# Optimization experiments

Measured on AMD Instinct MI355X. Metric: run time of the kernel, lower is better.

The kernel has to match this reference:

```python
import jax, jax.numpy as jnp
import numpy as np

D_MODEL = 1024
N_HEADS = 16
D_K = D_MODEL // N_HEADS


def setup_inputs() -> dict:
    key = jax.random.key(0)
    ks = jax.random.split(key, 5)
    x = jax.random.normal(ks[0], (4, 2048, D_MODEL), dtype=jnp.float32)
    # nn.Linear stores weight as [out, in]; we store transposed [in, out] for x @ W
    w_qkv = jax.random.normal(ks[1], (D_MODEL, 3 * D_MODEL), dtype=jnp.float32) / np.sqrt(D_MODEL)
    b_qkv = jnp.zeros((3 * D_MODEL,), dtype=jnp.float32)
    w_fc = jax.random.normal(ks[2], (D_MODEL, D_MODEL), dtype=jnp.float32) / np.sqrt(D_MODEL)
    b_fc = jnp.zeros((D_MODEL,), dtype=jnp.float32)
    ln_g = jnp.ones((D_MODEL,), dtype=jnp.float32)
    ln_b = jnp.zeros((D_MODEL,), dtype=jnp.float32)
    return {"x": x, "w_qkv": w_qkv, "b_qkv": b_qkv, "w_fc": w_fc, "b_fc": b_fc,
            "ln_g": ln_g, "ln_b": ln_b}


def _layernorm(x, g, b, eps=1e-5):
    mu = jnp.mean(x, axis=-1, keepdims=True)
    var = jnp.mean(jnp.square(x - mu), axis=-1, keepdims=True)
    return (x - mu) * jax.lax.rsqrt(var + eps) * g + b


def reference(x, w_qkv, b_qkv, w_fc, b_fc, ln_g, ln_b):
    residual = x
    xn = _layernorm(x, ln_g, ln_b)
    B, L, D = xn.shape
    qkv = xn @ w_qkv + b_qkv  # [B, L, 3D]
    q, k, v = jnp.split(qkv, 3, axis=-1)
    # b l (h d) -> b h l d
    def to_heads(t):
        return t.reshape(B, L, N_HEADS, D_K).transpose(0, 2, 1, 3)
    q, k, v = to_heads(q), to_heads(k), to_heads(v)
    scale = 1.0 / np.sqrt(D_K)
    scores = jnp.einsum('bhld,bhmd->bhlm', q, k) * scale  # [B,H,L,L]
    attn = jax.nn.softmax(scores, axis=-1)
    # dropout is identity in eval mode
    out = jnp.einsum('bhlm,bhmd->bhld', attn, v)  # [B,H,L,d]
    out = out.transpose(0, 2, 1, 3).reshape(B, L, D)  # b h l d -> b l (h d)
    out = out @ w_fc + b_fc
    return out + residual
```

## Files before the change

kernel.cpp:

```cpp
#include <hip/hip_runtime.h>
#include <hip/hip_bf16.h>
#include <cstdint>
#include <cstddef>

using bf16 = __hip_bfloat16;
typedef __attribute__((ext_vector_type(4))) float f32x4;
typedef __attribute__((ext_vector_type(8))) short bf16x8;

#define D_MODEL 1024
#define SEQ     2048
#define NB      4
#define NHEAD   16
#define DHEAD   64
#define NROWS   (NB * SEQ)

__device__ __forceinline__ void load_lds16(const void* g, void* l) {
  __builtin_amdgcn_global_load_lds(
      (const __attribute__((address_space(1))) unsigned int*)g,
      (__attribute__((address_space(3))) unsigned int*)l, 16, 0, 0);
}

__device__ __forceinline__ unsigned short f2bf(float f) {
  bf16 h = __float2bfloat16(f);
  return *(unsigned short*)&h;
}

__device__ __forceinline__ unsigned pk_trunc(float a, float b) {
  union { float f; unsigned u; } ca, cb;
  ca.f = a; cb.f = b;
  return (ca.u >> 16) | (cb.u & 0xffff0000u);
}

__global__ __launch_bounds__(256) void ln_kernel(
    const float* __restrict__ x, const float* __restrict__ g,
    const float* __restrict__ bb, bf16* __restrict__ xn) {
  int row  = blockIdx.x * 4 + (threadIdx.x >> 6);
  int lane = threadIdx.x & 63;
  const float4* xr = (const float4*)(x + (size_t)row * D_MODEL);
  float v[16], s = 0.f;
#pragma unroll
  for (int i = 0; i < 4; i++) {
    float4 t = xr[lane + 64 * i];
    v[4 * i] = t.x; v[4 * i + 1] = t.y; v[4 * i + 2] = t.z; v[4 * i + 3] = t.w;
    s += t.x + t.y + t.z + t.w;
  }
#pragma unroll
  for (int off = 32; off; off >>= 1) s += __shfl_xor(s, off, 64);
  float mean = s * (1.f / D_MODEL);
  float vs = 0.f;
#pragma unroll
  for (int i = 0; i < 16; i++) { float d = v[i] - mean; vs += d * d; }
#pragma unroll
  for (int off = 32; off; off >>= 1) vs += __shfl_xor(vs, off, 64);
  float rstd = rsqrtf(vs * (1.f / D_MODEL) + 1e-5f);
  ushort4* op = (ushort4*)(xn + (size_t)row * D_MODEL);
#pragma unroll
  for (int i = 0; i < 4; i++) {
    float4 gv = ((const float4*)g)[lane + 64 * i];
    float4 bv = ((const float4*)bb)[lane + 64 * i];
    ushort4 o;
    o.x = f2bf((v[4 * i]     - mean) * rstd * gv.x + bv.x);
    o.y = f2bf((v[4 * i + 1] - mean) * rstd * gv.y + bv.y);
    o.z = f2bf((v[4 * i + 2] - mean) * rstd * gv.z + bv.z);
    o.w = f2bf((v[4 * i + 3] - mean) * rstd * gv.w + bv.w);
    op[lane + 64 * i] = o;
  }
}

__global__ __launch_bounds__(256) void transpose_kernel(
    const float* __restrict__ w_qkv, bf16* __restrict__ wqkvT,
    const float* __restrict__ w_fc, bf16* __restrict__ wfcT) {
  __shared__ float tile[32][33];
  const float* in; bf16* out; int C, c0;
  if (blockIdx.x < 96) { in = w_qkv; out = wqkvT; C = 3072; c0 = blockIdx.x * 32; }
  else                 { in = w_fc;  out = wfcT;  C = 1024; c0 = (blockIdx.x - 96) * 32; }
  int r0 = blockIdx.y * 32;
  int tx = threadIdx.x & 31, ty = threadIdx.x >> 5;
  for (int i = ty; i < 32; i += 8)
    tile[i][tx] = in[(size_t)(r0 + i) * C + c0 + tx];
  __syncthreads();
  for (int i = ty; i < 32; i += 8)
    out[(size_t)(c0 + i) * 1024 + r0 + tx] = __float2bfloat16(tile[tx][i]);
}

__device__ __forceinline__ void store_ct(bf16* p, float v)  { *p = __float2bfloat16(v); }
__device__ __forceinline__ void store_ct(float* p, float v) { *p = v; }

template <int SPLIT, int RESID, typename CT>
__global__ __launch_bounds__(256) void gemm_bt(
    const bf16* __restrict__ A, const bf16* __restrict__ Bt,
    const float* __restrict__ bias, const float* __restrict__ resid,
    CT* __restrict__ C, bf16* __restrict__ vt, int M, int N, int K) {
  __shared__ __attribute__((aligned(16))) bf16 Alds[128 * 64];
  __shared__ __attribute__((aligned(16))) bf16 Blds[128 * 64];
  int tid = threadIdx.x, wave = tid >> 6, lane = tid & 63;
  int ntiles = N >> 7;
  int bm = blockIdx.x / ntiles, bn = blockIdx.x % ntiles;
  int m0 = bm << 7, n0 = bn << 7;
  int wm = (wave >> 1) << 6, wn = (wave & 1) << 6;
  int srow = tid >> 3;
  int sw8  = (((tid & 7) ^ (srow & 7)) << 3);
  int frow = lane & 15, quad = lane >> 4;
  const bf16* Ap[4];
  const bf16* Bp[4];
#pragma unroll
  for (int s = 0; s < 4; s++) {
    Ap[s] = A  + (size_t)(m0 + s * 32 + srow) * K + sw8;
    Bp[s] = Bt + (size_t)(n0 + s * 32 + srow) * K + sw8;
  }
  f32x4 acc[4][4] = {};
  for (int k0 = 0; k0 < K; k0 += 64) {
    __syncthreads();
#pragma unroll
    for (int s = 0; s < 4; s++) {
      load_lds16(Ap[s], (char*)Alds + s * 4096 + tid * 16);
      load_lds16(Bp[s], (char*)Blds + s * 4096 + tid * 16);
      Ap[s] += 64; Bp[s] += 64;
    }
    __syncthreads();
    bf16x8 af[4][2], bv[4][2];
#pragma unroll
    for (int i = 0; i < 4; i++)
#pragma unroll
      for (int kk = 0; kk < 2; kk++) {
        int e = (((kk * 4 + quad) ^ (frow & 7)) << 3);
        af[i][kk] = *(const bf16x8*)&Alds[(wm + i * 16 + frow) * 64 + e];
        bv[i][kk] = *(const bf16x8*)&Blds[(wn + i * 16 + frow) * 64 + e];
      }
#pragma unroll
    for (int i = 0; i < 4; i++)
#pragma unroll
      for (int j = 0; j < 4; j++) {
        acc[i][j] = __builtin_amdgcn_mfma_f32_16x16x32_bf16(af[i][0], bv[j][0], acc[i][j], 0, 0, 0);
        acc[i][j] = __builtin_amdgcn_mfma_f32_16x16x32_bf16(af[i][1], bv[j][1], acc[i][j], 0, 0, 0);
      }
  }
#pragma unroll
  for (int i = 0; i < 4; i++) {
    int row0 = m0 + wm + i * 16 + (quad << 2);
#pragma unroll
    for (int j = 0; j < 4; j++) {
      int col = n0 + wn + j * 16 + frow;
      float bvs = bias[col];
      if (SPLIT && col >= 2048) {
        int hd = col - 2048;
        int b = row0 >> 11, seq0 = row0 & 2047;
        int within = seq0 & 63, mt = within >> 4, q4 = (within >> 2) & 3;
        int pos = (seq0 & ~63) + ((mt >> 1) << 5) + (q4 << 3) + ((mt & 1) << 2);
        ushort4 pk;
        pk.x = f2bf(acc[i][j][0] + bvs);
        pk.y = f2bf(acc[i][j][1] + bvs);
        pk.z = f2bf(acc[i][j][2] + bvs);
        pk.w = f2bf(acc[i][j][3] + bvs);
        *(ushort4*)&vt[((size_t)(b * 1024 + hd)) * SEQ + pos] = pk;
      } else {
        int stride = SPLIT ? 2048 : N;
        float scale = (SPLIT && col < 1024) ? 0.18033688f : 1.0f;
#pragma unroll
        for (int r = 0; r < 4; r++) {
          size_t idx = (size_t)(row0 + r) * stride + col;
          float val = (acc[i][j][r] + bvs) * scale;
          if (RESID) val += resid[idx];
          store_ct(&C[idx], val);
        }
      }
    }
  }
}

__global__ __launch_bounds__(256, 4) void attn_kernel(
    const bf16* __restrict__ qk, const bf16* __restrict__ vt,
    bf16* __restrict__ aout) {
  int bh = blockIdx.x;
  int qt = blockIdx.y;
  int bb = bh >> 4, h = bh & 15;
  const bf16* Qg = qk + (size_t)bb * SEQ * 2048 + h * DHEAD;
  const bf16* Kg = Qg + D_MODEL;
  const bf16* Vg = vt + (size_t)bh * DHEAD * SEQ;

  __shared__ __attribute__((aligned(16))) bf16 Qlds[128 * 64];
  __shared__ __attribute__((aligned(16))) bf16 Klds[64 * 64];
  __shared__ __attribute__((aligned(16))) bf16 Vlds[64 * 64];

  int tid = threadIdx.x, wave = tid >> 6, lane = tid & 63;
  int prow = tid >> 3, pch = tid & 7;
  int lch8 = ((pch ^ (prow & 7)) << 3);
  int frow = lane & 15, quad = lane >> 4;
  int e0 = ((quad ^ (frow & 7)) << 3);
  int q0 = qt * 128;

#pragma unroll
  for (int s2 = 0; s2 < 4; s2++)
    load_lds16(Qg + (size_t)(q0 + s2 * 32 + prow) * 2048 + lch8,
               (char*)Qlds + s2 * 4096 + tid * 16);
  __syncthreads();
  bf16x8 qf[2][2];
#pragma unroll
  for (int qtile = 0; qtile < 2; qtile++)
#pragma unroll
    for (int kk = 0; kk < 2; kk++)
      qf[qtile][kk] =
          *(const bf16x8*)&Qlds[(wave * 32 + qtile * 16 + frow) * 64 + (e0 ^ (kk * 32))];

  f32x4 l4[2] = {};
  f32x4 o[4][2] = {};

  for (int kt = 0; kt < SEQ / 64; kt++) {
    int kv0 = kt * 64;
    __syncthreads();
#pragma unroll
    for (int s2 = 0; s2 < 2; s2++) {
      load_lds16(Kg + (size_t)(kv0 + s2 * 32 + prow) * 2048 + lch8,
                 (char*)Klds + s2 * 4096 + tid * 16);
      load_lds16(Vg + (size_t)(s2 * 32 + prow) * SEQ + kv0 + lch8,
                 (char*)Vlds + s2 * 4096 + tid * 16);
    }
    __syncthreads();

    f32x4 s[4][2] = {};
#pragma unroll
    for (int mt = 0; mt < 4; mt++) {
      bf16x8 af0 = *(const bf16x8*)&Klds[(mt * 16 + frow) * 64 + e0];
      bf16x8 af1 = *(const bf16x8*)&Klds[(mt * 16 + frow) * 64 + (e0 ^ 32)];
#pragma unroll
      for (int qtile = 0; qtile < 2; qtile++) {
        s[mt][qtile] = __builtin_amdgcn_mfma_f32_16x16x32_bf16(af0, qf[qtile][0], s[mt][qtile], 0, 0, 0);
        s[mt][qtile] = __builtin_amdgcn_mfma_f32_16x16x32_bf16(af1, qf[qtile][1], s[mt][qtile], 0, 0, 0);
      }
    }

    uint2 pk[2][4];
#pragma unroll
    for (int qtile = 0; qtile < 2; qtile++)
#pragma unroll
      for (int mt = 0; mt < 4; mt++) {
        f32x4 pv;
        pv[0] = __builtin_amdgcn_exp2f(s[mt][qtile][0]);
        pv[1] = __builtin_amdgcn_exp2f(s[mt][qtile][1]);
        pv[2] = __builtin_amdgcn_exp2f(s[mt][qtile][2]);
        pv[3] = __builtin_amdgcn_exp2f(s[mt][qtile][3]);
        l4[qtile] += pv;
        pk[qtile][mt].x = pk_trunc(pv[0], pv[1]);
        pk[qtile][mt].y = pk_trunc(pv[2], pv[3]);
      }

#pragma unroll
    for (int dt = 0; dt < 4; dt++) {
      bf16x8 vf0 = *(const bf16x8*)&Vlds[(dt * 16 + frow) * 64 + e0];
      bf16x8 vf1 = *(const bf16x8*)&Vlds[(dt * 16 + frow) * 64 + (e0 ^ 32)];
#pragma unroll
      for (int qtile = 0; qtile < 2; qtile++) {
        union { unsigned u[4]; bf16x8 v; } pf0, pf1;
        pf0.u[0] = pk[qtile][0].x; pf0.u[1] = pk[qtile][0].y;
        pf0.u[2] = pk[qtile][1].x; pf0.u[3] = pk[qtile][1].y;
        pf1.u[0] = pk[qtile][2].x; pf1.u[1] = pk[qtile][2].y;
        pf1.u[2] = pk[qtile][3].x; pf1.u[3] = pk[qtile][3].y;
        o[dt][qtile] = __builtin_amdgcn_mfma_f32_16x16x32_bf16(vf0, pf0.v, o[dt][qtile], 0, 0, 0);
        o[dt][qtile] = __builtin_amdgcn_mfma_f32_16x16x32_bf16(vf1, pf1.v, o[dt][qtile], 0, 0, 0);
      }
    }
  }

  float linv[2];
#pragma unroll
  for (int qtile = 0; qtile < 2; qtile++) {
    float v = (l4[qtile][0] + l4[qtile][1]) + (l4[qtile][2] + l4[qtile][3]);
    v += __shfl_xor(v, 16, 64);
    v += __shfl_xor(v, 32, 64);
    linv[qtile] = 1.f / v;
  }

  __syncthreads();
  bf16* Tw = (wave == 0) ? Qlds
           : (wave == 1) ? Qlds + 32 * 80
           : (wave == 2) ? Klds : Vlds;
#pragma unroll
  for (int qtile = 0; qtile < 2; qtile++)
#pragma unroll
    for (int dt = 0; dt < 4; dt++) {
      ushort4 pk;
      pk.x = f2bf(o[dt][qtile][0] * linv[qtile]);
      pk.y = f2bf(o[dt][qtile][1] * linv[qtile]);
      pk.z = f2bf(o[dt][qtile][2] * linv[qtile]);
      pk.w = f2bf(o[dt][qtile][3] * linv[qtile]);
      *(ushort4*)&Tw[(qtile * 16 + frow) * 80 + dt * 16 + quad * 4] = pk;
    }
  int rq = lane >> 1, d0 = (lane & 1) * 32;
  size_t grow = (size_t)(bb * SEQ + q0 + wave * 32 + rq);
#pragma unroll
  for (int i = 0; i < 4; i++) {
    bf16x8 v8 = *(const bf16x8*)&Tw[rq * 80 + d0 + i * 8];
    *(bf16x8*)&aout[grow * D_MODEL + h * DHEAD + d0 + i * 8] = v8;
  }
}

extern "C" void kernel_launch(void* const* d_in, const int* in_sizes, int n_in,
                              void* d_out, int out_size, void* d_ws, size_t ws_size,
                              hipStream_t stream) {
  const float* x     = (const float*)d_in[0];
  const float* w_qkv = (const float*)d_in[1];
  const float* b_qkv = (const float*)d_in[2];
  const float* w_fc  = (const float*)d_in[3];
  const float* b_fc  = (const float*)d_in[4];
  const float* ln_g  = (const float*)d_in[5];
  const float* ln_b  = (const float*)d_in[6];
  float* out = (float*)d_out;

  char* ws = (char*)d_ws;
  bf16* xn    = (bf16*)(ws);
  bf16* wqkvT = (bf16*)(ws + (16u << 20));
  bf16* wfcT  = (bf16*)(ws + (22u << 20));
  bf16* qk    = (bf16*)(ws + (24u << 20));
  bf16* vt    = (bf16*)(ws + (56u << 20));
  bf16* aout  = (bf16*)(ws);

  ln_kernel<<<NROWS / 4, 256, 0, stream>>>(x, ln_g, ln_b, xn);
  transpose_kernel<<<dim3(128, 32), 256, 0, stream>>>(w_qkv, wqkvT, w_fc, wfcT);
  gemm_bt<1, 0, bf16><<<(NROWS / 128) * (3 * D_MODEL / 128), 256, 0, stream>>>(
      xn, wqkvT, b_qkv, nullptr, qk, vt, NROWS, 3 * D_MODEL, D_MODEL);
  attn_kernel<<<dim3(NB * NHEAD, SEQ / 128), 256, 0, stream>>>(qk, vt, aout);
  gemm_bt<0, 1, float><<<(NROWS / 128) * (D_MODEL / 128), 256, 0, stream>>>(
      aout, wfcT, b_fc, x, out, nullptr, NROWS, D_MODEL, D_MODEL);
}
```

Measured before the change: 274.9 us.

## Double-buffer K/V tiles in attention kernel, reusing Q LDS as second buffer

Replaces the load-sync-compute loop with a two-stage ping-pong. The next K/V tile is issued via global_load_lds into an alternate buffer while the current tile is computed, and the Q shared-memory area is reused as the second buffer once Q fragments sit in registers. This aims to hide global load latency behind MFMA and exp work and halves the barriers per tile. It relies on async LDS loads completing before the next barrier, and adds address arithmetic plus a manually unrolled prologue and epilogue.

New measurement: 265.8 us. 3.3% less time.

```diff
diff --git a/kernel.cpp b/kernel.cpp
--- a/kernel.cpp
+++ b/kernel.cpp
@@ -168,6 +168,61 @@
   }
 }
 
+
+__device__ __forceinline__ void stage_kv(
+    const bf16* Kp0, const bf16* Kp1, const bf16* Vp0, const bf16* Vp1,
+    bf16* KB, bf16* VB, int tid) {
+  load_lds16(Kp0, (char*)KB + tid * 16);
+  load_lds16(Kp1, (char*)KB + 4096 + tid * 16);
+  load_lds16(Vp0, (char*)VB + tid * 16);
+  load_lds16(Vp1, (char*)VB + 4096 + tid * 16);
+}
+
+__device__ __forceinline__ void kv_tile(
+    const bf16* KL, const bf16* VL, int frow, int e0,
+    const bf16x8 (&qf)[2][2], f32x4 (&l4)[2], f32x4 (&o)[4][2]) {
+  f32x4 s[4][2] = {};
+#pragma unroll
+  for (int mt = 0; mt < 4; mt++) {
+    bf16x8 af0 = *(const bf16x8*)&KL[(mt * 16 + frow) * 64 + e0];
+    bf16x8 af1 = *(const bf16x8*)&KL[(mt * 16 + frow) * 64 + (e0 ^ 32)];
+#pragma unroll
+    for (int qt2 = 0; qt2 < 2; qt2++) {
+      s[mt][qt2] = __builtin_amdgcn_mfma_f32_16x16x32_bf16(af0, qf[qt2][0], s[mt][qt2], 0, 0, 0);
+      s[mt][qt2] = __builtin_amdgcn_mfma_f32_16x16x32_bf16(af1, qf[qt2][1], s[mt][qt2], 0, 0, 0);
+    }
+  }
+  uint2 pk[2][4];
+#pragma unroll
+  for (int qt2 = 0; qt2 < 2; qt2++)
+#pragma unroll
+    for (int mt = 0; mt < 4; mt++) {
+      f32x4 pv;
+      pv[0] = __builtin_amdgcn_exp2f(s[mt][qt2][0]);
+      pv[1] = __builtin_amdgcn_exp2f(s[mt][qt2][1]);
+      pv[2] = __builtin_amdgcn_exp2f(s[mt][qt2][2]);
+      pv[3] = __builtin_amdgcn_exp2f(s[mt][qt2][3]);
+      l4[qt2] += pv;
+      pk[qt2][mt].x = pk_trunc(pv[0], pv[1]);
+      pk[qt2][mt].y = pk_trunc(pv[2], pv[3]);
+    }
+#pragma unroll
+  for (int dt = 0; dt < 4; dt++) {
+    bf16x8 vf0 = *(const bf16x8*)&VL[(dt * 16 + frow) * 64 + e0];
+    bf16x8 vf1 = *(const bf16x8*)&VL[(dt * 16 + frow) * 64 + (e0 ^ 32)];
+#pragma unroll
+    for (int qt2 = 0; qt2 < 2; qt2++) {
+      union { unsigned u[4]; bf16x8 v; } pf0, pf1;
+      pf0.u[0] = pk[qt2][0].x; pf0.u[1] = pk[qt2][0].y;
+      pf0.u[2] = pk[qt2][1].x; pf0.u[3] = pk[qt2][1].y;
+      pf1.u[0] = pk[qt2][2].x; pf1.u[1] = pk[qt2][2].y;
+      pf1.u[2] = pk[qt2][3].x; pf1.u[3] = pk[qt2][3].y;
+      o[dt][qt2] = __builtin_amdgcn_mfma_f32_16x16x32_bf16(vf0, pf0.v, o[dt][qt2], 0, 0, 0);
+      o[dt][qt2] = __builtin_amdgcn_mfma_f32_16x16x32_bf16(vf1, pf1.v, o[dt][qt2], 0, 0, 0);
+    }
+  }
+}
+
 __global__ __launch_bounds__(256, 4) void attn_kernel(
     const bf16* __restrict__ qk, const bf16* __restrict__ vt,
     bf16* __restrict__ aout) {
@@ -189,6 +244,15 @@
   int e0 = ((quad ^ (frow & 7)) << 3);
   int q0 = qt * 128;
 
+  bf16* K0 = Klds;  bf16* V0 = Vlds;
+  bf16* K1 = Qlds;  bf16* V1 = Qlds + 64 * 64;
+
+  const bf16* Kp0 = Kg + (size_t)prow * 2048 + lch8;
+  const bf16* Kp1 = Kg + (size_t)(32 + prow) * 2048 + lch8;
+  const bf16* Vp0 = Vg + (size_t)prow * SEQ + lch8;
+  const bf16* Vp1 = Vg + (size_t)(32 + prow) * SEQ + lch8;
+  const size_t KT = (size_t)1 << 17;
+
 #pragma unroll
   for (int s2 = 0; s2 < 4; s2++)
     load_lds16(Qg + (size_t)(q0 + s2 * 32 + prow) * 2048 + lch8,
@@ -196,78 +260,39 @@
   __syncthreads();
   bf16x8 qf[2][2];
 #pragma unroll
-  for (int qtile = 0; qtile < 2; qtile++)
+  for (int qt2 = 0; qt2 < 2; qt2++)
 #pragma unroll
     for (int kk = 0; kk < 2; kk++)
-      qf[qtile][kk] =
-          *(const bf16x8*)&Qlds[(wave * 32 + qtile * 16 + frow) * 64 + (e0 ^ (kk * 32))];
+      qf[qt2][kk] =
+          *(const bf16x8*)&Qlds[(wave * 32 + qt2 * 16 + frow) * 64 + (e0 ^ (kk * 32))];
+  stage_kv(Kp0, Kp1, Vp0, Vp1, K0, V0, tid);
+  __syncthreads();
 
   f32x4 l4[2] = {};
   f32x4 o[4][2] = {};
 
-  for (int kt = 0; kt < SEQ / 64; kt++) {
-    int kv0 = kt * 64;
+#pragma unroll 1
+  for (int kt = 0; kt < 30; kt += 2) {
+    stage_kv(Kp0 + KT, Kp1 + KT, Vp0 + 64, Vp1 + 64, K1, V1, tid);
+    kv_tile(K0, V0, frow, e0, qf, l4, o);
     __syncthreads();
-#pragma unroll
-    for (int s2 = 0; s2 < 2; s2++) {
-      load_lds16(Kg + (size_t)(kv0 + s2 * 32 + prow) * 2048 + lch8,
-                 (char*)Klds + s2 * 4096 + tid * 16);
-      load_lds16(Vg + (size_t)(s2 * 32 + prow) * SEQ + kv0 + lch8,
-                 (char*)Vlds + s2 * 4096 + tid * 16);
-    }
+    stage_kv(Kp0 + 2 * KT, Kp1 + 2 * KT, Vp0 + 128, Vp1 + 128, K0, V0, tid);
+    kv_tile(K1, V1, frow, e0, qf, l4, o);
     __syncthreads();
-
-    f32x4 s[4][2] = {};
-#pragma unroll
-    for (int mt = 0; mt < 4; mt++) {
-      bf16x8 af0 = *(const bf16x8*)&Klds[(mt * 16 + frow) * 64 + e0];
-      bf16x8 af1 = *(const bf16x8*)&Klds[(mt * 16 + frow) * 64 + (e0 ^ 32)];
-#pragma unroll
-      for (int qtile = 0; qtile < 2; qtile++) {
-        s[mt][qtile] = __builtin_amdgcn_mfma_f32_16x16x32_bf16(af0, qf[qtile][0], s[mt][qtile], 0, 0, 0);
-        s[mt][qtile] = __builtin_amdgcn_mfma_f32_16x16x32_bf16(af1, qf[qtile][1], s[mt][qtile], 0, 0, 0);
-      }
-    }
-
-    uint2 pk[2][4];
-#pragma unroll
-    for (int qtile = 0; qtile < 2; qtile++)
-#pragma unroll
-      for (int mt = 0; mt < 4; mt++) {
-        f32x4 pv;
-        pv[0] = __builtin_amdgcn_exp2f(s[mt][qtile][0]);
-        pv[1] = __builtin_amdgcn_exp2f(s[mt][qtile][1]);
-        pv[2] = __builtin_amdgcn_exp2f(s[mt][qtile][2]);
-        pv[3] = __builtin_amdgcn_exp2f(s[mt][qtile][3]);
-        l4[qtile] += pv;
-        pk[qtile][mt].x = pk_trunc(pv[0], pv[1]);
-        pk[qtile][mt].y = pk_trunc(pv[2], pv[3]);
-      }
-
-#pragma unroll
-    for (int dt = 0; dt < 4; dt++) {
-      bf16x8 vf0 = *(const bf16x8*)&Vlds[(dt * 16 + frow) * 64 + e0];
-      bf16x8 vf1 = *(const bf16x8*)&Vlds[(dt * 16 + frow) * 64 + (e0 ^ 32)];
-#pragma unroll
-      for (int qtile = 0; qtile < 2; qtile++) {
-        union { unsigned u[4]; bf16x8 v; } pf0, pf1;
-        pf0.u[0] = pk[qtile][0].x; pf0.u[1] = pk[qtile][0].y;
-        pf0.u[2] = pk[qtile][1].x; pf0.u[3] = pk[qtile][1].y;
-        pf1.u[0] = pk[qtile][2].x; pf1.u[1] = pk[qtile][2].y;
-        pf1.u[2] = pk[qtile][3].x; pf1.u[3] = pk[qtile][3].y;
-        o[dt][qtile] = __builtin_amdgcn_mfma_f32_16x16x32_bf16(vf0, pf0.v, o[dt][qtile], 0, 0, 0);
-        o[dt][qtile] = __builtin_amdgcn_mfma_f32_16x16x32_bf16(vf1, pf1.v, o[dt][qtile], 0, 0, 0);
-      }
-    }
-  }
+    Kp0 += 2 * KT; Kp1 += 2 * KT; Vp0 += 128; Vp1 += 128;
+  }
+  stage_kv(Kp0 + KT, Kp1 + KT, Vp0 + 64, Vp1 + 64, K1, V1, tid);
+  kv_tile(K0, V0, frow, e0, qf, l4, o);
+  __syncthreads();
+  kv_tile(K1, V1, frow, e0, qf, l4, o);
 
   float linv[2];
 #pragma unroll
-  for (int qtile = 0; qtile < 2; qtile++) {
-    float v = (l4[qtile][0] + l4[qtile][1]) + (l4[qtile][2] + l4[qtile][3]);
+  for (int qt2 = 0; qt2 < 2; qt2++) {
+    float v = (l4[qt2][0] + l4[qt2][1]) + (l4[qt2][2] + l4[qt2][3]);
     v += __shfl_xor(v, 16, 64);
     v += __shfl_xor(v, 32, 64);
-    linv[qtile] = 1.f / v;
+    linv[qt2] = 1.f / v;
   }
 
   __syncthreads();
@@ -275,15 +300,15 @@
            : (wave == 1) ? Qlds + 32 * 80
            : (wave == 2) ? Klds : Vlds;
 #pragma unroll
-  for (int qtile = 0; qtile < 2; qtile++)
+  for (int qt2 = 0; qt2 < 2; qt2++)
 #pragma unroll
     for (int dt = 0; dt < 4; dt++) {
       ushort4 pk;
-      pk.x = f2bf(o[dt][qtile][0] * linv[qtile]);
-      pk.y = f2bf(o[dt][qtile][1] * linv[qtile]);
-      pk.z = f2bf(o[dt][qtile][2] * linv[qtile]);
-      pk.w = f2bf(o[dt][qtile][3] * linv[qtile]);
-      *(ushort4*)&Tw[(qtile * 16 + frow) * 80 + dt * 16 + quad * 4] = pk;
+      pk.x = f2bf(o[dt][qt2][0] * linv[qt2]);
+      pk.y = f2bf(o[dt][qt2][1] * linv[qt2]);
+      pk.z = f2bf(o[dt][qt2][2] * linv[qt2]);
+      pk.w = f2bf(o[dt][qt2][3] * linv[qt2]);
+      *(ushort4*)&Tw[(qt2 * 16 + frow) * 80 + dt * 16 + quad * 4] = pk;
     }
   int rq = lane >> 1, d0 = (lane & 1) * 32;
   size_t grow = (size_t)(bb * SEQ + q0 + wave * 32 + rq);
```
